# Kernel optimization log

Measured on AMD Instinct MI355X. Metric: run time of the kernel, lower is better.

Reference implementation:

```python
import jax, jax.numpy as jnp
import numpy as np

L1 = 3072
L2 = 15
L3 = 32
COUNT = 8
KAN_G = 3   # grid intervals
KAN_K = 3   # spline order


def _bspline_basis(x, grid, k):
    """Cox-de Boor B-spline basis. x: [B, in], grid: [in, G+2k+1] -> [B, in, G+k]."""
    x = x[:, :, None]                      # [B, in, 1]
    g = grid[None]                         # [1, in, M]
    B0 = ((x >= g[:, :, :-1]) & (x < g[:, :, 1:])).astype(x.dtype)
    for d in range(1, k + 1):
        B0 = ((x - g[:, :, : -(d + 1)]) / (g[:, :, d:-1] - g[:, :, : -(d + 1)]) * B0[:, :, :-1]
              + (g[:, :, d + 1:] - x) / (g[:, :, d + 1:] - g[:, :, 1:-d]) * B0[:, :, 1:])
    return B0  # [B, in, G+k]


def setup_inputs() -> dict:
    key = jax.random.key(0)
    ks = jax.random.split(key, 9)
    B = 16384
    in_dim = L2 * 2            # 30
    out_dim = L3 * COUNT       # 256
    x = jax.random.normal(ks[0], (B, L1), jnp.float32) * 0.1
    ls_indices = jax.random.randint(ks[1], (B,), 0, COUNT, dtype=jnp.int32)
    l1_w = jax.random.normal(ks[2], ((L2 + 1) * COUNT, L1), jnp.float32) / np.sqrt(L1).astype(np.float32)
    l1_b = jax.random.normal(ks[3], ((L2 + 1) * COUNT,), jnp.float32) * 0.01
    l1f_w = jax.random.normal(ks[4], (L2 + 1, L1), jnp.float32) / np.sqrt(L1).astype(np.float32)
    l1f_b = jnp.zeros((L2 + 1,), jnp.float32)
    # KAN layer: uniform extended grid on [-1,1], G+2k+1 = 10 knots per input dim
    h = 2.0 / KAN_G
    g1 = jnp.arange(-KAN_K, KAN_G + KAN_K + 1, dtype=jnp.float32) * h - 1.0
    kan_grid = jnp.tile(g1[None], (in_dim, 1))                      # [30, 10]
    kan_coef = jax.random.normal(ks[5], (in_dim, out_dim, KAN_G + KAN_K), jnp.float32) * 0.1
    kan_scale_base = jax.random.normal(ks[6], (in_dim, out_dim), jnp.float32) / np.sqrt(in_dim).astype(np.float32)
    kan_scale_sp = jnp.ones((in_dim, out_dim), jnp.float32)
    out_w = jax.random.normal(ks[7], (COUNT, L3), jnp.float32) / np.sqrt(L3).astype(np.float32)
    out_b = jnp.zeros((COUNT,), jnp.float32)
    return dict(x=x, ls_indices=ls_indices, l1_w=l1_w, l1_b=l1_b, l1f_w=l1f_w, l1f_b=l1f_b,
                kan_grid=kan_grid, kan_coef=kan_coef, kan_scale_base=kan_scale_base,
                kan_scale_sp=kan_scale_sp, out_w=out_w, out_b=out_b)


def reference(x, ls_indices, l1_w, l1_b, l1f_w, l1f_b, kan_grid, kan_coef,
              kan_scale_base, kan_scale_sp, out_w, out_b):
    B = x.shape[0]
    idx = ls_indices.reshape(-1) + jnp.arange(B, dtype=ls_indices.dtype) * COUNT  # [B]
    # l1: dense over all stacks, then gather the selected stack row per sample
    l1s = (x @ l1_w.T + l1_b).reshape(B * COUNT, L2 + 1)
    l1c = l1s[idx]                                  # [B, L2+1]
    l1f = x @ l1f_w.T + l1f_b                       # [B, L2+1]
    l1c_, l1c_out = l1c[:, :L2], l1c[:, L2:]
    l1f_, l1f_out = l1f[:, :L2], l1f[:, L2:]
    l1x = l1c_ + l1f_                               # [B, L2]
    l1x = jnp.clip(jnp.concatenate([l1x * l1x * (127.0 / 128.0), l1x], axis=1), 0.0, 1.0)  # [B, 2*L2]
    # KAN layer (single KANLayer, 30 -> 256): silu base + B-spline, summed over inputs
    basis = _bspline_basis(l1x, kan_grid, KAN_K)    # [B, 30, G+k]
    w_sp = kan_coef * kan_scale_sp[:, :, None]      # fold scale into coef -> [30, 256, G+k]
    l2s = (jnp.einsum('bi,io->bo', jax.nn.silu(l1x), kan_scale_base)
           + jnp.einsum('bik,iok->bo', basis, w_sp))  # [B, 256]
    l2c = l2s.reshape(B * COUNT, L3)[idx]           # [B, L3]
    l2x = jnp.clip(l2c, 0.0, 1.0)
    l3s = (l2x @ out_w.T + out_b).reshape(B * COUNT, 1)
    l3c = l3s[idx]                                  # [B, 1]
    return l3c + l1f_out + l1c_out
```

## Files before the change

### kernel.cpp

```cpp
#include <hip/hip_runtime.h>
#include <hip/hip_bf16.h>
#include <math.h>

#define NB 16384
#define KD 3072
#define TPB 256
#define CAP 2560
#define BPB 80

typedef __attribute__((ext_vector_type(8))) short bf16x8;
typedef __attribute__((ext_vector_type(4))) float f32x4;

#define WS_IDX_OFF 64
#define WS_W_OFF 82048
#define WS_WK_OFF 966784

__device__ __forceinline__ unsigned short f2bf(float f) {
    unsigned u = __float_as_uint(f);
    u += 0x7FFFu + ((u >> 16) & 1u);
    return (unsigned short)(u >> 16);
}

__device__ __forceinline__ unsigned pk2(float a, float b) {
    float2 t; t.x = a; t.y = b;
    __hip_bfloat162 h = __float22bfloat162_rn(t);
    return *(unsigned*)&h;
}

__global__ void k_pre(const float* __restrict__ l1_w, const float* __restrict__ l1f_w,
                      unsigned short* __restrict__ W,
                      const float* __restrict__ coef, const float* __restrict__ sb,
                      const float* __restrict__ sp, unsigned short* __restrict__ Wk,
                      const int* __restrict__ ls, int* __restrict__ meta) {
    int bid = blockIdx.x;
    int tid = threadIdx.x;
    if (bid < 432) {
        int g = bid * TPB + tid;
        int e = g * 4;
        const float* src = (e < 128 * KD) ? (l1_w + e) : (l1f_w + (e - 128 * KD));
        float4 v = *(const float4*)src;
        int2 o;
        o.x = (unsigned)f2bf(v.x) | ((unsigned)f2bf(v.y) << 16);
        o.y = (unsigned)f2bf(v.z) | ((unsigned)f2bf(v.w) << 16);
        *(int2*)(W + e) = o;
    } else if (bid < 688) {
        int o = bid - 432;
        int k = tid;
        if (k < 224) {
            float val = 0.f;
            if (k < 30) {
                val = sb[k * 256 + o];
            } else if (k >= 32 && k < 212) {
                int t = k - 32;
                int i = t / 6;
                int kk = t - i * 6;
                val = coef[((size_t)i * 256 + o) * 6 + kk] * sp[i * 256 + o];
            }
            Wk[o * 224 + k] = f2bf(val);
        }
    } else {
        int j = bid - 688;
        int r = j * TPB + tid;
        int bb = ls[r];
        int lane = tid & 63;
        int* idxL = meta + 16;
        for (int qq = 0; qq < 8; qq++) {
            unsigned long long mask = __ballot(bb == qq);
            if (mask != 0ull) {
                int leader = __ffsll((unsigned long long)mask) - 1;
                int base = 0;
                if (lane == leader) base = atomicAdd(&meta[qq], (int)__popcll(mask));
                base = __shfl(base, leader);
                if (bb == qq) {
                    int rank = (int)__popcll(mask & ((1ull << lane) - 1ull));
                    int pos = base + rank;
                    if (pos < CAP) idxL[qq * CAP + pos] = r;
                }
            }
        }
    }
}

__global__ __launch_bounds__(TPB, 4) void k2_main(
    const float* __restrict__ x, const int* __restrict__ meta,
    const unsigned short* __restrict__ W, const unsigned short* __restrict__ WkG,
    const float* __restrict__ l1_b, const float* __restrict__ l1f_b,
    const float* __restrict__ out_w, const float* __restrict__ out_b,
    float* __restrict__ out)
{
    __shared__ int s_rows[32];
    __shared__ int s_valid[32];
    __shared__ float hS[32][33];
    __shared__ float sPart[2][32];
    __shared__ char smem[34816];

    unsigned short* Abuf = (unsigned short*)smem;
    unsigned short* Bbuf = (unsigned short*)(smem + 17408);
    unsigned short* uL   = (unsigned short*)smem;
    unsigned short* WkS  = (unsigned short*)(smem + 14848);

    int tid = threadIdx.x;
    int q = blockIdx.x / BPB;
    int rel0 = (blockIdx.x - q * BPB) * 32;
    int cnt = meta[q]; if (cnt > CAP) cnt = CAP;
    if (rel0 >= cnt) return;
    const int* idxL = meta + 16;
    if (tid < 32) {
        int rel = rel0 + tid;
        int valid = (rel < cnt) ? 1 : 0;
        s_rows[tid] = idxL[q * CAP + (valid ? rel : 0)];
        s_valid[tid] = valid;
    }
    __syncthreads();

    int w = tid >> 6, lane = tid & 63;
    int mt = w & 1, nt = w >> 1;
    int quad = lane >> 4, l16 = lane & 15;
    int sm = tid >> 3, seg = tid & 7;

    const float4* xp = (const float4*)(x + (size_t)s_rows[sm] * KD) + seg * 4;
    int wrow = (sm < 16) ? (q * 16 + sm) : (112 + sm);
    const int4* wp = (const int4*)(W + (size_t)wrow * KD) + seg * 2;

    int wrA = sm * 136 + seg * 16;
    int arow = mt * 16 + l16, brow = nt * 16 + l16;
    int rdA = arow * 136, rdB = brow * 136;

    float4 xa0 = xp[0], xa1 = xp[1], xa2 = xp[2], xa3 = xp[3];
    int4 wv0 = wp[0], wv1 = wp[1];

    f32x4 acc = {0.f, 0.f, 0.f, 0.f};
    for (int kt = 0; kt < 24; kt++) {
        int4 a0, a1, b0i = wv0, b1i = wv1;
        a0.x = pk2(xa0.x, xa0.y); a0.y = pk2(xa0.z, xa0.w);
        a0.z = pk2(xa1.x, xa1.y); a0.w = pk2(xa1.z, xa1.w);
        a1.x = pk2(xa2.x, xa2.y); a1.y = pk2(xa2.z, xa2.w);
        a1.z = pk2(xa3.x, xa3.y); a1.w = pk2(xa3.z, xa3.w);
        if (kt < 23) {
            xa0 = xp[(kt + 1) * 32];     xa1 = xp[(kt + 1) * 32 + 1];
            xa2 = xp[(kt + 1) * 32 + 2]; xa3 = xp[(kt + 1) * 32 + 3];
            wv0 = wp[(kt + 1) * 16];     wv1 = wp[(kt + 1) * 16 + 1];
        }
        unsigned short* ab = Abuf + (kt & 1) * 4352;
        unsigned short* bb = Bbuf + (kt & 1) * 4352;
        *(int4*)(ab + wrA) = a0;  *(int4*)(ab + wrA + 8) = a1;
        *(int4*)(bb + wrA) = b0i; *(int4*)(bb + wrA + 8) = b1i;
        __syncthreads();
#pragma unroll
        for (int ks = 0; ks < 4; ks++) {
            bf16x8 af  = *(const bf16x8*)(ab + rdA + ks * 32 + quad * 8);
            bf16x8 bfv = *(const bf16x8*)(bb + rdB + ks * 32 + quad * 8);
            acc = __builtin_amdgcn_mfma_f32_16x16x32_bf16(af, bfv, acc, 0, 0, 0);
        }
    }

    {
        int col = nt * 16 + l16;
        float bias = (col < 16) ? l1_b[q * 16 + col] : l1f_b[col - 16];
        int rbase = mt * 16 + quad * 4;
        hS[rbase + 0][col] = acc[0] + bias;
        hS[rbase + 1][col] = acc[1] + bias;
        hS[rbase + 2][col] = acc[2] + bias;
        hS[rbase + 3][col] = acc[3] + bias;
    }
    __syncthreads();

    if (tid < 32) {
        unsigned* z = (unsigned*)(uL + tid * 232 + 212);
        z[0] = 0; z[1] = 0; z[2] = 0; z[3] = 0; z[4] = 0; z[5] = 0;
        *(unsigned*)(uL + tid * 232 + 30) = 0;
    }
    for (int item = tid; item < 480; item += TPB) {
        int row = item / 15;
        int ii = item - row * 15;
        float v = hS[row][ii] + hS[row][16 + ii];
        float xs = fminf(v * v * (127.f / 128.f), 1.f);
        float xl = fminf(fmaxf(v, 0.f), 1.f);
#pragma unroll
        for (int which = 0; which < 2; which++) {
            float xv = which ? xl : xs;
            int i = which ? (15 + ii) : ii;
            float sg = 1.f / (1.f + __expf(-xv));
            uL[row * 232 + i] = f2bf(xv * sg);
            float s = xv * 1.5f + 4.5f;
            int j = (int)s;
            float f = s - (float)j;
            float omf = 1.f - f;
            float f2 = f * f, f3 = f2 * f;
            float N0 = omf * omf * omf * (1.f / 6.f);
            float N1 = (3.f * f3 - 6.f * f2 + 4.f) * (1.f / 6.f);
            float N2 = (-3.f * f3 + 3.f * f2 + 3.f * f + 1.f) * (1.f / 6.f);
            float N3 = f3 * (1.f / 6.f);
            float b1 = (j == 4) ? N0 : 0.f;
            float b2 = (j == 4) ? N1 : ((j == 5) ? N0 : 0.f);
            float b3 = (j == 4) ? N2 : ((j == 5) ? N1 : N0);
            float b4 = (j == 4) ? N3 : ((j == 5) ? N2 : N1);
            float b5 = (j == 5) ? N3 : ((j == 6) ? N2 : 0.f);
            unsigned* dst = (unsigned*)(uL + row * 232 + 32 + i * 6);
            dst[0] = ((unsigned)f2bf(b1) << 16);
            dst[1] = (unsigned)f2bf(b2) | ((unsigned)f2bf(b3) << 16);
            dst[2] = (unsigned)f2bf(b4) | ((unsigned)f2bf(b5) << 16);
        }
    }
    for (int c = tid; c < 448; c += TPB) {
        int row = c / 14;
        int cc = c - row * 14;
        const int4* src = (const int4*)(WkG + ((size_t)(q * 32 + row)) * 224 + cc * 16);
        int4 v0 = src[0];
        int4 v1 = src[1];
        int4* dst = (int4*)(WkS + row * 232 + cc * 16);
        dst[0] = v0;
        dst[1] = v1;
    }
    __syncthreads();

    f32x4 acc2 = {0.f, 0.f, 0.f, 0.f};
    const unsigned short* uRd = uL + (mt * 16 + l16) * 232 + quad * 8;
    const unsigned short* wRd = WkS + (nt * 16 + l16) * 232 + quad * 8;
#pragma unroll
    for (int ks = 0; ks < 7; ks++) {
        bf16x8 uf = *(const bf16x8*)(uRd + ks * 32);
        bf16x8 wf = *(const bf16x8*)(wRd + ks * 32);
        acc2 = __builtin_amdgcn_mfma_f32_16x16x32_bf16(uf, wf, acc2, 0, 0, 0);
    }

    float ow = out_w[q * 32 + nt * 16 + l16];
    float p0 = fminf(fmaxf(acc2[0], 0.f), 1.f) * ow;
    float p1 = fminf(fmaxf(acc2[1], 0.f), 1.f) * ow;
    float p2 = fminf(fmaxf(acc2[2], 0.f), 1.f) * ow;
    float p3 = fminf(fmaxf(acc2[3], 0.f), 1.f) * ow;
#pragma unroll
    for (int off = 1; off < 16; off <<= 1) {
        p0 += __shfl_xor(p0, off);
        p1 += __shfl_xor(p1, off);
        p2 += __shfl_xor(p2, off);
        p3 += __shfl_xor(p3, off);
    }
    if (l16 == 0) {
        int rbase = mt * 16 + quad * 4;
        sPart[nt][rbase + 0] = p0;
        sPart[nt][rbase + 1] = p1;
        sPart[nt][rbase + 2] = p2;
        sPart[nt][rbase + 3] = p3;
    }
    __syncthreads();
    if (tid < 32 && s_valid[tid]) {
        float res = sPart[0][tid] + sPart[1][tid] + out_b[q] + hS[tid][15] + hS[tid][31];
        out[s_rows[tid]] = res;
    }
}

extern "C" void kernel_launch(void* const* d_in, const int* in_sizes, int n_in,
                              void* d_out, int out_size, void* d_ws, size_t ws_size,
                              hipStream_t stream) {
    (void)in_sizes; (void)n_in; (void)out_size; (void)ws_size;
    const float* x     = (const float*)d_in[0];
    const int*   ls    = (const int*)d_in[1];
    const float* l1_w  = (const float*)d_in[2];
    const float* l1_b  = (const float*)d_in[3];
    const float* l1f_w = (const float*)d_in[4];
    const float* l1f_b = (const float*)d_in[5];
    const float* coef  = (const float*)d_in[7];
    const float* sb    = (const float*)d_in[8];
    const float* sp    = (const float*)d_in[9];
    const float* ow    = (const float*)d_in[10];
    const float* ob    = (const float*)d_in[11];
    float* out = (float*)d_out;

    char* ws = (char*)d_ws;
    int* meta = (int*)ws;
    unsigned short* W  = (unsigned short*)(ws + WS_W_OFF);
    unsigned short* Wk = (unsigned short*)(ws + WS_WK_OFF);

    hipMemsetAsync(meta, 0, 64, stream);
    hipLaunchKernelGGL(k_pre, dim3(752), dim3(TPB), 0, stream,
                       l1_w, l1f_w, W, coef, sb, sp, Wk, ls, meta);
    hipLaunchKernelGGL(k2_main, dim3(8 * BPB), dim3(TPB), 0, stream,
                       x, meta, W, Wk, l1_b, l1f_b, ow, ob, out);
}
```

Before: 340.3 us.

## Use single-wave 16-row tiles loading MFMA fragments directly from global memory

The main kernel drops from 256-thread blocks over 32 rows to 64-thread single-wave blocks over 16 rows, doubling the grid. Operands are loaded straight from global memory into registers in MFMA fragment layout, double-buffered, which removes the LDS staging and the per-k-step block barriers. The KAN weights are also read directly from global memory rather than copied to LDS. The risk is less reuse of W and x per block, uncoalesced 16-byte strided global loads, and higher register pressure.

```diff
diff --git a/kernel.cpp b/kernel.cpp
--- a/kernel.cpp
+++ b/kernel.cpp
@@ -6,12 +6,12 @@
 #define KD 3072
 #define TPB 256
 #define CAP 2560
-#define BPB 80
+#define K2B 64
+#define BPB 160
 
 typedef __attribute__((ext_vector_type(8))) short bf16x8;
 typedef __attribute__((ext_vector_type(4))) float f32x4;
 
-#define WS_IDX_OFF 64
 #define WS_W_OFF 82048
 #define WS_WK_OFF 966784
 
@@ -81,172 +81,192 @@
     }
 }
 
-__global__ __launch_bounds__(TPB, 4) void k2_main(
+__global__ __launch_bounds__(K2B, 2) void k2_main(
     const float* __restrict__ x, const int* __restrict__ meta,
-    const unsigned short* __restrict__ W, const unsigned short* __restrict__ WkG,
+    const unsigned short* __restrict__ W, const unsigned short* __restrict__ Wk,
     const float* __restrict__ l1_b, const float* __restrict__ l1f_b,
     const float* __restrict__ out_w, const float* __restrict__ out_b,
     float* __restrict__ out)
 {
-    __shared__ int s_rows[32];
-    __shared__ int s_valid[32];
-    __shared__ float hS[32][33];
-    __shared__ float sPart[2][32];
-    __shared__ char smem[34816];
-
-    unsigned short* Abuf = (unsigned short*)smem;
-    unsigned short* Bbuf = (unsigned short*)(smem + 17408);
-    unsigned short* uL   = (unsigned short*)smem;
-    unsigned short* WkS  = (unsigned short*)(smem + 14848);
+    __shared__ float hS[16][33];
+    __shared__ unsigned short uL[16][232];
 
     int tid = threadIdx.x;
     int q = blockIdx.x / BPB;
-    int rel0 = (blockIdx.x - q * BPB) * 32;
+    int rel0 = (blockIdx.x - q * BPB) * 16;
     int cnt = meta[q]; if (cnt > CAP) cnt = CAP;
     if (rel0 >= cnt) return;
     const int* idxL = meta + 16;
-    if (tid < 32) {
+    int myrow = 0, myvalid = 0;
+    if (tid < 16) {
         int rel = rel0 + tid;
-        int valid = (rel < cnt) ? 1 : 0;
-        s_rows[tid] = idxL[q * CAP + (valid ? rel : 0)];
-        s_valid[tid] = valid;
+        myvalid = (rel < cnt) ? 1 : 0;
+        myrow = idxL[q * CAP + (myvalid ? rel : 0)];
+    }
+    int l16 = tid & 15, quad = tid >> 4;
+    int arow = __shfl(myrow, l16);
+
+    const float* aP = x + (size_t)arow * KD + quad * 8;
+    const unsigned short* b0P = W + (size_t)(q * 16 + l16) * KD + quad * 8;
+    const unsigned short* b1P = W + (size_t)(128 + l16) * KD + quad * 8;
+
+    f32x4 acc0 = {0.f, 0.f, 0.f, 0.f};
+    f32x4 acc1 = {0.f, 0.f, 0.f, 0.f};
+
+    float4 ca[8]; int4 cb0[4], cb1[4];
+    float4 na[8]; int4 nb0[4], nb1[4];
+#pragma unroll
+    for (int s = 0; s < 4; s++) {
+        ca[2 * s]     = *(const float4*)(aP + s * 32);
+        ca[2 * s + 1] = *(const float4*)(aP + s * 32 + 4);
+        cb0[s] = *(const int4*)(b0P + s * 32);
+        cb1[s] = *(const int4*)(b1P + s * 32);
+    }
+    for (int kt = 0; kt < 24; kt += 2) {
+        {
+            const float* ap = aP + (kt + 1) * 128;
+            const unsigned short* p0 = b0P + (kt + 1) * 128;
+            const unsigned short* p1 = b1P + (kt + 1) * 128;
+#pragma unroll
+            for (int s = 0; s < 4; s++) {
+                na[2 * s]     = *(const float4*)(ap + s * 32);
+                na[2 * s + 1] = *(const float4*)(ap + s * 32 + 4);
+                nb0[s] = *(const int4*)(p0 + s * 32);
+                nb1[s] = *(const int4*)(p1 + s * 32);
+            }
+        }
+#pragma unroll
+        for (int s = 0; s < 4; s++) {
+            int4 ai;
+            ai.x = pk2(ca[2 * s].x, ca[2 * s].y);
+            ai.y = pk2(ca[2 * s].z, ca[2 * s].w);
+            ai.z = pk2(ca[2 * s + 1].x, ca[2 * s + 1].y);
+            ai.w = pk2(ca[2 * s + 1].z, ca[2 * s + 1].w);
+            bf16x8 af = *(bf16x8*)&ai;
+            acc0 = __builtin_amdgcn_mfma_f32_16x16x32_bf16(af, *(bf16x8*)&cb0[s], acc0, 0, 0, 0);
+            acc1 = __builtin_amdgcn_mfma_f32_16x16x32_bf16(af, *(bf16x8*)&cb1[s], acc1, 0, 0, 0);
+        }
+        if (kt < 22) {
+            const float* ap = aP + (kt + 2) * 128;
+            const unsigned short* p0 = b0P + (kt + 2) * 128;
+            const unsigned short* p1 = b1P + (kt + 2) * 128;
+#pragma unroll
+            for (int s = 0; s < 4; s++) {
+                ca[2 * s]     = *(const float4*)(ap + s * 32);
+                ca[2 * s + 1] = *(const float4*)(ap + s * 32 + 4);
+                cb0[s] = *(const int4*)(p0 + s * 32);
+                cb1[s] = *(const int4*)(p1 + s * 32);
+            }
+        }
+#pragma unroll
+        for (int s = 0; s < 4; s++) {
+            int4 ai;
+            ai.x = pk2(na[2 * s].x, na[2 * s].y);
+            ai.y = pk2(na[2 * s].z, na[2 * s].w);
+            ai.z = pk2(na[2 * s + 1].x, na[2 * s + 1].y);
+            ai.w = pk2(na[2 * s + 1].z, na[2 * s + 1].w);
+            bf16x8 af = *(bf16x8*)&ai;
+            acc0 = __builtin_amdgcn_mfma_f32_16x16x32_bf16(af, *(bf16x8*)&nb0[s], acc0, 0, 0, 0);
+            acc1 = __builtin_amdgcn_mfma_f32_16x16x32_bf16(af, *(bf16x8*)&nb1[s], acc1, 0, 0, 0);
+        }
+    }
+
+    {
+        float bsel = l1_b[q * 16 + l16];
+        float bff  = l1f_b[l16];
+#pragma unroll
+        for (int r = 0; r < 4; r++) {
+            hS[quad * 4 + r][l16]      = acc0[r] + bsel;
+            hS[quad * 4 + r][16 + l16] = acc1[r] + bff;
+        }
     }
     __syncthreads();
 
-    int w = tid >> 6, lane = tid & 63;
-    int mt = w & 1, nt = w >> 1;
-    int quad = lane >> 4, l16 = lane & 15;
-    int sm = tid >> 3, seg = tid & 7;
-
-    const float4* xp = (const float4*)(x + (size_t)s_rows[sm] * KD) + seg * 4;
-    int wrow = (sm < 16) ? (q * 16 + sm) : (112 + sm);
-    const int4* wp = (const int4*)(W + (size_t)wrow * KD) + seg * 2;
-
-    int wrA = sm * 136 + seg * 16;
-    int arow = mt * 16 + l16, brow = nt * 16 + l16;
-    int rdA = arow * 136, rdB = brow * 136;
-
-    float4 xa0 = xp[0], xa1 = xp[1], xa2 = xp[2], xa3 = xp[3];
-    int4 wv0 = wp[0], wv1 = wp[1];
-
-    f32x4 acc = {0.f, 0.f, 0.f, 0.f};
-    for (int kt = 0; kt < 24; kt++) {
-        int4 a0, a1, b0i = wv0, b1i = wv1;
-        a0.x = pk2(xa0.x, xa0.y); a0.y = pk2(xa0.z, xa0.w);
-        a0.z = pk2(xa1.x, xa1.y); a0.w = pk2(xa1.z, xa1.w);
-        a1.x = pk2(xa2.x, xa2.y); a1.y = pk2(xa2.z, xa2.w);
-        a1.z = pk2(xa3.x, xa3.y); a1.w = pk2(xa3.z, xa3.w);
-        if (kt < 23) {
-            xa0 = xp[(kt + 1) * 32];     xa1 = xp[(kt + 1) * 32 + 1];
-            xa2 = xp[(kt + 1) * 32 + 2]; xa3 = xp[(kt + 1) * 32 + 3];
-            wv0 = wp[(kt + 1) * 16];     wv1 = wp[(kt + 1) * 16 + 1];
-        }
-        unsigned short* ab = Abuf + (kt & 1) * 4352;
-        unsigned short* bb = Bbuf + (kt & 1) * 4352;
-        *(int4*)(ab + wrA) = a0;  *(int4*)(ab + wrA + 8) = a1;
-        *(int4*)(bb + wrA) = b0i; *(int4*)(bb + wrA + 8) = b1i;
-        __syncthreads();
-#pragma unroll
-        for (int ks = 0; ks < 4; ks++) {
-            bf16x8 af  = *(const bf16x8*)(ab + rdA + ks * 32 + quad * 8);
-            bf16x8 bfv = *(const bf16x8*)(bb + rdB + ks * 32 + quad * 8);
-            acc = __builtin_amdgcn_mfma_f32_16x16x32_bf16(af, bfv, acc, 0, 0, 0);
-        }
-    }
-
+#pragma unroll
+    for (int t = 0; t < 4; t++) {
+        int it = tid + 64 * t;
+        if (it < 240) {
+            int i = it >> 4;
+            int m = it & 15;
+            float v = hS[m][i] + hS[m][16 + i];
+            float xs = fminf(v * v * (127.f / 128.f), 1.f);
+            float xl = fminf(fmaxf(v, 0.f), 1.f);
+#pragma unroll
+            for (int which = 0; which < 2; which++) {
+                float xv = which ? xl : xs;
+                int ii = which ? (15 + i) : i;
+                float sg = 1.f / (1.f + __expf(-xv));
+                uL[m][ii] = f2bf(xv * sg);
+                float s = xv * 1.5f + 4.5f;
+                int j = (int)s;
+                float f = s - (float)j;
+                float omf = 1.f - f;
+                float f2 = f * f, f3 = f2 * f;
+                float N0 = omf * omf * omf * (1.f / 6.f);
+                float N1 = (3.f * f3 - 6.f * f2 + 4.f) * (1.f / 6.f);
+                float N2 = (-3.f * f3 + 3.f * f2 + 3.f * f + 1.f) * (1.f / 6.f);
+                float N3 = f3 * (1.f / 6.f);
+                float b1 = (j == 4) ? N0 : 0.f;
+                float b2 = (j == 4) ? N1 : ((j == 5) ? N0 : 0.f);
+                float b3 = (j == 4) ? N2 : ((j == 5) ? N1 : N0);
+                float b4 = (j == 4) ? N3 : ((j == 5) ? N2 : N1);
+                float b5 = (j == 5) ? N3 : ((j == 6) ? N2 : 0.f);
+                unsigned* dst = (unsigned*)&uL[m][32 + ii * 6];
+                dst[0] = ((unsigned)f2bf(b1) << 16);
+                dst[1] = (unsigned)f2bf(b2) | ((unsigned)f2bf(b3) << 16);
+                dst[2] = (unsigned)f2bf(b4) | ((unsigned)f2bf(b5) << 16);
+            }
+        }
+    }
+    if (tid < 16) {
+        *(unsigned*)&uL[tid][30] = 0;
+        unsigned* z = (unsigned*)&uL[tid][212];
+        z[0] = 0; z[1] = 0; z[2] = 0; z[3] = 0; z[4] = 0; z[5] = 0;
+    }
+    __syncthreads();
+
+    f32x4 acc2a = {0.f, 0.f, 0.f, 0.f};
+    f32x4 acc2b = {0.f, 0.f, 0.f, 0.f};
     {
-        int col = nt * 16 + l16;
-        float bias = (col < 16) ? l1_b[q * 16 + col] : l1f_b[col - 16];
-        int rbase = mt * 16 + quad * 4;
-        hS[rbase + 0][col] = acc[0] + bias;
-        hS[rbase + 1][col] = acc[1] + bias;
-        hS[rbase + 2][col] = acc[2] + bias;
-        hS[rbase + 3][col] = acc[3] + bias;
-    }
-    __syncthreads();
-
-    if (tid < 32) {
-        unsigned* z = (unsigned*)(uL + tid * 232 + 212);
-        z[0] = 0; z[1] = 0; z[2] = 0; z[3] = 0; z[4] = 0; z[5] = 0;
-        *(unsigned*)(uL + tid * 232 + 30) = 0;
-    }
-    for (int item = tid; item < 480; item += TPB) {
-        int row = item / 15;
-        int ii = item - row * 15;
-        float v = hS[row][ii] + hS[row][16 + ii];
-        float xs = fminf(v * v * (127.f / 128.f), 1.f);
-        float xl = fminf(fmaxf(v, 0.f), 1.f);
-#pragma unroll
-        for (int which = 0; which < 2; which++) {
-            float xv = which ? xl : xs;
-            int i = which ? (15 + ii) : ii;
-            float sg = 1.f / (1.f + __expf(-xv));
-            uL[row * 232 + i] = f2bf(xv * sg);
-            float s = xv * 1.5f + 4.5f;
-            int j = (int)s;
-            float f = s - (float)j;
-            float omf = 1.f - f;
-            float f2 = f * f, f3 = f2 * f;
-            float N0 = omf * omf * omf * (1.f / 6.f);
-            float N1 = (3.f * f3 - 6.f * f2 + 4.f) * (1.f / 6.f);
-            float N2 = (-3.f * f3 + 3.f * f2 + 3.f * f + 1.f) * (1.f / 6.f);
-            float N3 = f3 * (1.f / 6.f);
-            float b1 = (j == 4) ? N0 : 0.f;
-            float b2 = (j == 4) ? N1 : ((j == 5) ? N0 : 0.f);
-            float b3 = (j == 4) ? N2 : ((j == 5) ? N1 : N0);
-            float b4 = (j == 4) ? N3 : ((j == 5) ? N2 : N1);
-            float b5 = (j == 5) ? N3 : ((j == 6) ? N2 : 0.f);
-            unsigned* dst = (unsigned*)(uL + row * 232 + 32 + i * 6);
-            dst[0] = ((unsigned)f2bf(b1) << 16);
-            dst[1] = (unsigned)f2bf(b2) | ((unsigned)f2bf(b3) << 16);
-            dst[2] = (unsigned)f2bf(b4) | ((unsigned)f2bf(b5) << 16);
-        }
-    }
-    for (int c = tid; c < 448; c += TPB) {
-        int row = c / 14;
-        int cc = c - row * 14;
-        const int4* src = (const int4*)(WkG + ((size_t)(q * 32 + row)) * 224 + cc * 16);
-        int4 v0 = src[0];
-        int4 v1 = src[1];
-        int4* dst = (int4*)(WkS + row * 232 + cc * 16);
-        dst[0] = v0;
-        dst[1] = v1;
-    }
-    __syncthreads();
-
-    f32x4 acc2 = {0.f, 0.f, 0.f, 0.f};
-    const unsigned short* uRd = uL + (mt * 16 + l16) * 232 + quad * 8;
-    const unsigned short* wRd = WkS + (nt * 16 + l16) * 232 + quad * 8;
-#pragma unroll
-    for (int ks = 0; ks < 7; ks++) {
-        bf16x8 uf = *(const bf16x8*)(uRd + ks * 32);
-        bf16x8 wf = *(const bf16x8*)(wRd + ks * 32);
-        acc2 = __builtin_amdgcn_mfma_f32_16x16x32_bf16(uf, wf, acc2, 0, 0, 0);
-    }
-
-    float ow = out_w[q * 32 + nt * 16 + l16];
-    float p0 = fminf(fmaxf(acc2[0], 0.f), 1.f) * ow;
-    float p1 = fminf(fmaxf(acc2[1], 0.f), 1.f) * ow;
-    float p2 = fminf(fmaxf(acc2[2], 0.f), 1.f) * ow;
-    float p3 = fminf(fmaxf(acc2[3], 0.f), 1.f) * ow;
+        const unsigned short* uP  = &uL[l16][quad * 8];
+        const unsigned short* k0P = Wk + (size_t)(q * 32 + l16) * 224 + quad * 8;
+        const unsigned short* k1P = Wk + (size_t)(q * 32 + 16 + l16) * 224 + quad * 8;
+#pragma unroll
+        for (int ks = 0; ks < 7; ks++) {
+            bf16x8 uf = *(const bf16x8*)(uP + ks * 32);
+            acc2a = __builtin_amdgcn_mfma_f32_16x16x32_bf16(uf, *(const bf16x8*)(k0P + ks * 32), acc2a, 0, 0, 0);
+            acc2b = __builtin_amdgcn_mfma_f32_16x16x32_bf16(uf, *(const bf16x8*)(k1P + ks * 32), acc2b, 0, 0, 0);
+        }
+    }
+
+    float ow0 = out_w[q * 32 + l16];
+    float ow1 = out_w[q * 32 + 16 + l16];
+    float p[4];
+#pragma unroll
+    for (int r = 0; r < 4; r++) {
+        p[r] = fminf(fmaxf(acc2a[r], 0.f), 1.f) * ow0
+             + fminf(fmaxf(acc2b[r], 0.f), 1.f) * ow1;
+    }
 #pragma unroll
     for (int off = 1; off < 16; off <<= 1) {
-        p0 += __shfl_xor(p0, off);
-        p1 += __shfl_xor(p1, off);
-        p2 += __shfl_xor(p2, off);
-        p3 += __shfl_xor(p3, off);
+        p[0] += __shfl_xor(p[0], off);
+        p[1] += __shfl_xor(p[1], off);
+        p[2] += __shfl_xor(p[2], off);
+        p[3] += __shfl_xor(p[3], off);
+    }
+    int rowm[4], valm[4];
+#pragma unroll
+    for (int r = 0; r < 4; r++) {
+        rowm[r] = __shfl(myrow, quad * 4 + r);
+        valm[r] = __shfl(myvalid, quad * 4 + r);
     }
     if (l16 == 0) {
-        int rbase = mt * 16 + quad * 4;
-        sPart[nt][rbase + 0] = p0;
-        sPart[nt][rbase + 1] = p1;
-        sPart[nt][rbase + 2] = p2;
-        sPart[nt][rbase + 3] = p3;
-    }
-    __syncthreads();
-    if (tid < 32 && s_valid[tid]) {
-        float res = sPart[0][tid] + sPart[1][tid] + out_b[q] + hS[tid][15] + hS[tid][31];
-        out[s_rows[tid]] = res;
+        float obq = out_b[q];
+#pragma unroll
+        for (int r = 0; r < 4; r++) {
+            int m = quad * 4 + r;
+            if (valm[r]) out[rowm[r]] = p[r] + obq + hS[m][15] + hS[m][31];
+        }
     }
 }
 
@@ -275,6 +295,6 @@
     hipMemsetAsync(meta, 0, 64, stream);
     hipLaunchKernelGGL(k_pre, dim3(752), dim3(TPB), 0, stream,
                        l1_w, l1f_w, W, coef, sb, sp, Wk, ls, meta);
-    hipLaunchKernelGGL(k2_main, dim3(8 * BPB), dim3(TPB), 0, stream,
+    hipLaunchKernelGGL(k2_main, dim3(8 * BPB), dim3(K2B), 0, stream,
                        x, meta, W, Wk, l1_b, l1f_b, ow, ob, out);
 }
```

New measurement: 344.4 us. Within noise of the previous version (+1.2%).
